# Performance work log

Measured on AMD Instinct MI355X. Metric: run time of the kernel, lower is better.

## Reference

```python
import jax, jax.numpy as jnp
import numpy as np
from jax import lax

IN, H1, H2, F1, OUT = 26, 64, 32, 16, 10
B, T = 512, 1000


def _lstm(x, w_ih, w_hh, b_ih, b_hh):
    """PyTorch-convention LSTM (gate order i,f,g,o). x: [B,T,I].
    Returns (all hidden states [B,T,H], final hidden [B,H])."""
    Bx = x.shape[0]
    H = w_hh.shape[1]
    # Precompute input projections for all timesteps: [B,T,4H]
    xg = jnp.einsum('bti,gi->btg', x, w_ih) + b_ih + b_hh

    def step(carry, xg_t):
        h, c = carry
        gates = xg_t + h @ w_hh.T  # [B,4H]
        i, f, g, o = jnp.split(gates, 4, axis=-1)
        i = jax.nn.sigmoid(i)
        f = jax.nn.sigmoid(f)
        g = jnp.tanh(g)
        o = jax.nn.sigmoid(o)
        c = f * c + i * g
        h = o * jnp.tanh(c)
        return (h, c), h

    init = (jnp.zeros((Bx, H), x.dtype), jnp.zeros((Bx, H), x.dtype))
    (h_last, _), hs = lax.scan(step, init, xg.transpose(1, 0, 2))
    return hs.transpose(1, 0, 2), h_last


def setup_inputs() -> dict:
    key = jax.random.key(0)
    ks = jax.random.split(key, 14)

    def u(k, shape, fan):
        bound = 1.0 / np.sqrt(fan)
        return jax.random.uniform(k, shape, jnp.float32, -bound, bound)

    return {
        'x': jax.random.normal(ks[0], (B, 1, IN, T), jnp.float32),
        'w_ih1': u(ks[1], (4 * H1, IN), H1),
        'w_hh1': u(ks[2], (4 * H1, H1), H1),
        'b_ih1': u(ks[3], (4 * H1,), H1),
        'b_hh1': u(ks[4], (4 * H1,), H1),
        'w_ih2': u(ks[5], (4 * H2, H1), H2),
        'w_hh2': u(ks[6], (4 * H2, H2), H2),
        'b_ih2': u(ks[7], (4 * H2,), H2),
        'b_hh2': u(ks[8], (4 * H2,), H2),
        'w_fc1': u(ks[9], (F1, H2), H2),
        'b_fc1': u(ks[10], (F1,), H2),
        'w_fc2': u(ks[11], (OUT, F1), F1),
        'b_fc2': u(ks[12], (OUT,), F1),
    }


def reference(x, w_ih1, w_hh1, b_ih1, b_hh1, w_ih2, w_hh2, b_ih2, b_hh2,
              w_fc1, b_fc1, w_fc2, b_fc2):
    # [B,1,26,T] -> [B,26,T] -> [B,T,26]
    x = jnp.transpose(x[:, 0], (0, 2, 1))
    out1, _ = _lstm(x, w_ih1, w_hh1, b_ih1, b_hh1)
    # Dropout is identity in eval mode.
    _, h2 = _lstm(out1, w_ih2, w_hh2, b_ih2, b_hh2)  # final hidden [B,32]
    h = jax.nn.relu(h2 @ w_fc1.T + b_fc1)
    return h @ w_fc2.T + b_fc2  # [B,10]
```

## Files before the change

kernel.cpp:

```cpp
#include <hip/hip_runtime.h>
#include <hip/hip_bf16.h>


typedef __hip_bfloat16 bf16;
typedef _Float16 h2v __attribute__((ext_vector_type(2)));

#define T_STEPS 1000
#define IN_DIM  26

__device__ __forceinline__ float bits2f(unsigned short h) {
    unsigned int u = ((unsigned int)h) << 16;
    return __uint_as_float(u);
}

__device__ __forceinline__ float ldv(const void* p, int idx, bool isb) {
    return isb ? bits2f(((const unsigned short*)p)[idx])
               : ((const float*)p)[idx];
}

__device__ __forceinline__ float sigm(float x) {
    return 1.0f / (1.0f + __expf(-x));
}

__device__ __forceinline__ float tanh_(float x) {
    float a = fabsf(x);
    float e = __expf(2.0f * a);
    float r = 1.0f - 2.0f / (e + 1.0f);
    return copysignf(r, x);
}

__device__ __forceinline__ float DOT2(h2v a, h2v b, float c) {
    return __builtin_amdgcn_fdot2(a, b, c, false);
}

__device__ __forceinline__ h2v pkh(float a, float b) {
    h2v r; r[0] = (_Float16)a; r[1] = (_Float16)b; return r;
}

__device__ __forceinline__ h2v f2h2(float f) {
    return __builtin_bit_cast(h2v, f);
}

__global__
__attribute__((amdgpu_flat_work_group_size(128, 128), amdgpu_waves_per_eu(1, 1)))
void lstm_fused(const void* __restrict__ x,
                const void* __restrict__ w_ih1, const void* __restrict__ w_hh1,
                const void* __restrict__ b_ih1, const void* __restrict__ b_hh1,
                const void* __restrict__ w_ih2, const void* __restrict__ w_hh2,
                const void* __restrict__ b_ih2, const void* __restrict__ b_hh2,
                const void* __restrict__ w_fc1, const void* __restrict__ b_fc1,
                const void* __restrict__ w_fc2, const void* __restrict__ b_fc2,
                void* __restrict__ out)
{
    const int j    = threadIdx.x;
    const int wid  = j >> 6;
    const int lane = j & 63;
    const int e    = blockIdx.x;
    const long xbase = (long)e * (IN_DIM * T_STEPS);

    __shared__ __align__(16) _Float16 xsh[2][32];
    __shared__ __align__(16) _Float16 h1sh[2][64];
    __shared__ __align__(16) _Float16 h2sh[32];
    __shared__ __align__(16) float4   xgshf[2][64];
    __shared__ __align__(16) float    f1s[16];

    bool isb = true;
    {
        const unsigned short* wu = (const unsigned short*)w_ih1;
        for (int k = 0; k < 64; ++k) {
            float v = fabsf(bits2f(wu[k]));
            if (!(v <= 0.1251f)) isb = false;
        }
    }

    if (wid == 0) {
        h1sh[0][lane] = (_Float16)0.f;
        h1sh[1][lane] = (_Float16)0.f;

        h2v w1h[4][32];
#pragma unroll
        for (int r = 0; r < 4; ++r) {
            const int row = r * 64 + lane;
#pragma unroll
            for (int q = 0; q < 32; ++q)
                w1h[r][q] = pkh(ldv(w_hh1, row * 64 + 2 * q, isb),
                                ldv(w_hh1, row * 64 + 2 * q + 1, isb));
        }
        __syncthreads();

        float c1 = 0.f;
        for (int s = 0; s <= T_STEPS; ++s) {
            if (s < T_STEPS) {
                const int cur = s & 1, prv = cur ^ 1;
                float4 xg = xgshf[cur][lane];
                float4 hb[8];
                {
                    const float4* hp = (const float4*)h1sh[prv];
#pragma unroll
                    for (int q = 0; q < 8; ++q) hb[q] = hp[q];
                }
                const float* hbf = (const float*)hb;
                float acc[4][2] = {{0.f,0.f},{0.f,0.f},{0.f,0.f},{0.f,0.f}};
#pragma unroll
                for (int q = 0; q < 32; ++q) {
                    h2v hv = f2h2(hbf[q]);
#pragma unroll
                    for (int r = 0; r < 4; ++r)
                        acc[r][q & 1] = DOT2(w1h[r][q], hv, acc[r][q & 1]);
                }
                float pi = acc[0][0] + acc[0][1] + xg.x;
                float pf = acc[1][0] + acc[1][1] + xg.y;
                float pg = acc[2][0] + acc[2][1] + xg.z;
                float po = acc[3][0] + acc[3][1] + xg.w;
                float gi = sigm(pi), gf = sigm(pf), gg = tanh_(pg), go = sigm(po);
                c1 = fmaf(gf, c1, gi * gg);
                h1sh[cur][lane] = (_Float16)(go * tanh_(c1));
            }
            __syncthreads();
        }
    } else {
        h2v w1x[4][13];
        float bias1v[4];
#pragma unroll
        for (int r = 0; r < 4; ++r) {
            const int row = r * 64 + lane;
#pragma unroll
            for (int q = 0; q < 13; ++q)
                w1x[r][q] = pkh(ldv(w_ih1, row * 26 + 2 * q, isb),
                                ldv(w_ih1, row * 26 + 2 * q + 1, isb));
            bias1v[r] = ldv(b_ih1, row, isb) + ldv(b_hh1, row, isb);
        }
        const int u2 = lane & 31;
        const int lo = (lane < 32) ? 1 : 0;
        const int rA2 = (lo ? 0 : 32) + u2;
        const int rB2 = 64 + (lo ? 0 : 32) + u2;
        h2v w2x[2][32], w2h[2][16];
        float bias2v[2];
#pragma unroll
        for (int rr = 0; rr < 2; ++rr) {
            const int row = rr ? rB2 : rA2;
#pragma unroll
            for (int q = 0; q < 32; ++q)
                w2x[rr][q] = pkh(ldv(w_ih2, row * 64 + 2 * q, isb),
                                 ldv(w_ih2, row * 64 + 2 * q + 1, isb));
#pragma unroll
            for (int q = 0; q < 16; ++q)
                w2h[rr][q] = pkh(ldv(w_hh2, row * 32 + 2 * q, isb),
                                 ldv(w_hh2, row * 32 + 2 * q + 1, isb));
            bias2v[rr] = ldv(b_ih2, row, isb) + ldv(b_hh2, row, isb);
        }

        if (lane < 32) {
            h2sh[lane] = (_Float16)0.f;
            xsh[0][lane] = (_Float16)0.f;
            xsh[1][lane] = (_Float16)0.f;
        }
        if (lane < IN_DIM) {
            xsh[0][lane] = (_Float16)ldv(x, xbase + lane * T_STEPS + 0, isb);
            xsh[1][lane] = (_Float16)ldv(x, xbase + lane * T_STEPS + 1, isb);
        }
        {
            float4 xb[4];
            const float4* xp = (const float4*)xsh[0];
#pragma unroll
            for (int q = 0; q < 4; ++q) xb[q] = xp[q];
            const float* xbf = (const float*)xb;
            float ax[4][2] = {{0.f,0.f},{0.f,0.f},{0.f,0.f},{0.f,0.f}};
#pragma unroll
            for (int q = 0; q < 13; ++q) {
                h2v xv = f2h2(xbf[q]);
#pragma unroll
                for (int r = 0; r < 4; ++r)
                    ax[r][q & 1] = DOT2(w1x[r][q], xv, ax[r][q & 1]);
            }
            float4 xg;
            xg.x = ax[0][0] + ax[0][1] + bias1v[0];
            xg.y = ax[1][0] + ax[1][1] + bias1v[1];
            xg.z = ax[2][0] + ax[2][1] + bias1v[2];
            xg.w = ax[3][0] + ax[3][1] + bias1v[3];
            xgshf[0][lane] = xg;
        }
        __syncthreads();

        float c2 = 0.f;
        for (int s = 0; s <= T_STEPS; ++s) {
            float px = 0.f;
            const bool doPf = (s + 2 < T_STEPS) && (lane < IN_DIM);
            if (doPf) px = ldv(x, xbase + lane * T_STEPS + (s + 2), isb);

            if (s + 1 < T_STEPS) {
                const int nb = (s + 1) & 1;
                float4 xb[4];
                const float4* xp = (const float4*)xsh[nb];
#pragma unroll
                for (int q = 0; q < 4; ++q) xb[q] = xp[q];
                const float* xbf = (const float*)xb;
                float ax[4][2] = {{0.f,0.f},{0.f,0.f},{0.f,0.f},{0.f,0.f}};
#pragma unroll
                for (int q = 0; q < 13; ++q) {
                    h2v xv = f2h2(xbf[q]);
#pragma unroll
                    for (int r = 0; r < 4; ++r)
                        ax[r][q & 1] = DOT2(w1x[r][q], xv, ax[r][q & 1]);
                }
                float4 xg;
                xg.x = ax[0][0] + ax[0][1] + bias1v[0];
                xg.y = ax[1][0] + ax[1][1] + bias1v[1];
                xg.z = ax[2][0] + ax[2][1] + bias1v[2];
                xg.w = ax[3][0] + ax[3][1] + bias1v[3];
                xgshf[nb][lane] = xg;
            }

            if (s >= 1) {
                const int hb1 = (s + 1) & 1;
                float4 hb[8];
                {
                    const float4* hp = (const float4*)h1sh[hb1];
#pragma unroll
                    for (int q = 0; q < 8; ++q) hb[q] = hp[q];
                }
                const float* hbf = (const float*)hb;
                float4 pb[4];
                {
                    const float4* pp = (const float4*)h2sh;
#pragma unroll
                    for (int q = 0; q < 4; ++q) pb[q] = pp[q];
                }
                const float* pbf = (const float*)pb;
                float a2[2][2] = {{0.f,0.f},{0.f,0.f}};
#pragma unroll
                for (int q = 0; q < 32; ++q) {
                    h2v hv = f2h2(hbf[q]);
#pragma unroll
                    for (int rr = 0; rr < 2; ++rr)
                        a2[rr][q & 1] = DOT2(w2x[rr][q], hv, a2[rr][q & 1]);
                }
#pragma unroll
                for (int q = 0; q < 16; ++q) {
                    h2v pv = f2h2(pbf[q]);
#pragma unroll
                    for (int rr = 0; rr < 2; ++rr)
                        a2[rr][q & 1] = DOT2(w2h[rr][q], pv, a2[rr][q & 1]);
                }
                float pA = a2[0][0] + a2[0][1] + bias2v[0];
                float pB = a2[1][0] + a2[1][1] + bias2v[1];
                float actA = sigm(pA);
                float actB = lo ? tanh_(pB) : sigm(pB);
                float other = __shfl_xor(
                    __builtin_bit_cast(float, pkh(actA, actB)), 32, 64);
                if (lo) {
                    h2v fo = __builtin_bit_cast(h2v, other);
                    c2 = fmaf((float)fo[0], c2, actA * actB);
                    h2sh[u2] = (_Float16)((float)fo[1] * tanh_(c2));
                }
            }

            if (doPf) xsh[s & 1][lane] = (_Float16)px;

            __syncthreads();
        }

        if (lane < 16) {
            float ss = ldv(b_fc1, lane, isb);
#pragma unroll
            for (int k = 0; k < 32; ++k)
                ss = fmaf(ldv(w_fc1, lane * 32 + k, isb), (float)h2sh[k], ss);
            f1s[lane] = fmaxf(ss, 0.0f);
        }
        if (lane < 10) {
            float ss = ldv(b_fc2, lane, isb);
#pragma unroll
            for (int k = 0; k < 16; ++k)
                ss = fmaf(ldv(w_fc2, lane * 16 + k, isb), f1s[k], ss);
            const int oidx = e * 10 + lane;
            if (isb) ((bf16*)out)[oidx] = __float2bfloat16(ss);
            else     ((float*)out)[oidx] = ss;
        }
    }
}

extern "C" void kernel_launch(void* const* d_in, const int* in_sizes, int n_in,
                              void* d_out, int out_size, void* d_ws, size_t ws_size,
                              hipStream_t stream) {
    lstm_fused<<<dim3(512), dim3(128), 0, stream>>>(
        d_in[0], d_in[1], d_in[2], d_in[3], d_in[4],
        d_in[5], d_in[6], d_in[7], d_in[8],
        d_in[9], d_in[10], d_in[11], d_in[12], d_out);
}
```

Baseline: 913.3 us.

## Batch 16 sequences per block and compute LSTM gates with MFMA

```diff
diff --git a/kernel.cpp b/kernel.cpp
--- a/kernel.cpp
+++ b/kernel.cpp
@@ -3,46 +3,37 @@
 
 
 typedef __hip_bfloat16 bf16;
-typedef _Float16 h2v __attribute__((ext_vector_type(2)));
+typedef _Float16 f16;
+typedef _Float16 f16x8 __attribute__((ext_vector_type(8)));
+typedef _Float16 f16x4 __attribute__((ext_vector_type(4)));
+typedef float    f32x4 __attribute__((ext_vector_type(4)));
 
 #define T_STEPS 1000
 #define IN_DIM  26
+#define EPB     16
+#define CH      16
+#define H1P     72
+#define H2P     40
 
 __device__ __forceinline__ float bits2f(unsigned short h) {
-    unsigned int u = ((unsigned int)h) << 16;
-    return __uint_as_float(u);
-}
-
-__device__ __forceinline__ float ldv(const void* p, int idx, bool isb) {
-    return isb ? bits2f(((const unsigned short*)p)[idx])
-               : ((const float*)p)[idx];
-}
-
+    return __uint_as_float(((unsigned int)h) << 16);
+}
+__device__ __forceinline__ float ldv(const void* p, long i, bool isb) {
+    return isb ? bits2f(((const unsigned short*)p)[i]) : ((const float*)p)[i];
+}
+__device__ __forceinline__ float rcp_(float x) { return __builtin_amdgcn_rcpf(x); }
 __device__ __forceinline__ float sigm(float x) {
-    return 1.0f / (1.0f + __expf(-x));
-}
-
+    return rcp_(1.0f + __expf(-x));
+}
 __device__ __forceinline__ float tanh_(float x) {
     float a = fabsf(x);
-    float e = __expf(2.0f * a);
-    float r = 1.0f - 2.0f / (e + 1.0f);
+    float r = 1.0f - 2.0f * rcp_(__expf(2.0f * a) + 1.0f);
     return copysignf(r, x);
 }
-
-__device__ __forceinline__ float DOT2(h2v a, h2v b, float c) {
-    return __builtin_amdgcn_fdot2(a, b, c, false);
-}
-
-__device__ __forceinline__ h2v pkh(float a, float b) {
-    h2v r; r[0] = (_Float16)a; r[1] = (_Float16)b; return r;
-}
-
-__device__ __forceinline__ h2v f2h2(float f) {
-    return __builtin_bit_cast(h2v, f);
-}
+#define MFMA(a, b, c) __builtin_amdgcn_mfma_f32_16x16x32_f16((a), (b), (c), 0, 0, 0)
 
 __global__
-__attribute__((amdgpu_flat_work_group_size(128, 128), amdgpu_waves_per_eu(1, 1)))
+__attribute__((amdgpu_flat_work_group_size(256, 256), amdgpu_waves_per_eu(1, 1)))
 void lstm_fused(const void* __restrict__ x,
                 const void* __restrict__ w_ih1, const void* __restrict__ w_hh1,
                 const void* __restrict__ b_ih1, const void* __restrict__ b_hh1,
@@ -52,17 +43,17 @@
                 const void* __restrict__ w_fc2, const void* __restrict__ b_fc2,
                 void* __restrict__ out)
 {
-    const int j    = threadIdx.x;
-    const int wid  = j >> 6;
-    const int lane = j & 63;
-    const int e    = blockIdx.x;
-    const long xbase = (long)e * (IN_DIM * T_STEPS);
-
-    __shared__ __align__(16) _Float16 xsh[2][32];
-    __shared__ __align__(16) _Float16 h1sh[2][64];
-    __shared__ __align__(16) _Float16 h2sh[32];
-    __shared__ __align__(16) float4   xgshf[2][64];
-    __shared__ __align__(16) float    f1s[16];
+    const int tid  = threadIdx.x;
+    const int lane = tid & 63;
+    const int wv   = tid >> 6;
+    const int ecol = lane & 15;
+    const int g4   = lane >> 4;
+    const int e0   = blockIdx.x * EPB;
+
+    __shared__ __align__(16) f16  Xst[2][CH][EPB][32];
+    __shared__ __align__(16) f16  H1T[2][EPB][H1P];
+    __shared__ __align__(16) f16  H2T[2][EPB][H2P];
+    __shared__ __align__(16) float f1s[EPB][16];
 
     bool isb = true;
     {
@@ -73,216 +64,171 @@
         }
     }
 
-    if (wid == 0) {
-        h1sh[0][lane] = (_Float16)0.f;
-        h1sh[1][lane] = (_Float16)0.f;
-
-        h2v w1h[4][32];
-#pragma unroll
-        for (int r = 0; r < 4; ++r) {
-            const int row = r * 64 + lane;
-#pragma unroll
-            for (int q = 0; q < 32; ++q)
-                w1h[r][q] = pkh(ldv(w_hh1, row * 64 + 2 * q, isb),
-                                ldv(w_hh1, row * 64 + 2 * q + 1, isb));
-        }
+    {
+        float4 z; z.x = z.y = z.z = z.w = 0.f;
+        float4* p = (float4*)&Xst[0][0][0][0];
+        for (int k = tid; k < (int)(sizeof(Xst) / 16); k += 256) p[k] = z;
+        float4* q = (float4*)&H1T[0][0][0];
+        for (int k = tid; k < (int)(sizeof(H1T) / 16); k += 256) q[k] = z;
+        float4* r = (float4*)&H2T[0][0][0];
+        for (int k = tid; k < (int)(sizeof(H2T) / 16); k += 256) r[k] = z;
+    }
+
+    const int r15 = lane & 15;
+    f16x8 Whh1A[4][2], Wih1A[4];
+    f32x4 b1C[4];
+#pragma unroll
+    for (int gi = 0; gi < 4; ++gi) {
+        const int R = gi * 64 + 16 * wv + r15;
+#pragma unroll
+        for (int k0 = 0; k0 < 2; ++k0)
+#pragma unroll
+            for (int jj = 0; jj < 8; ++jj)
+                Whh1A[gi][k0][jj] =
+                    (f16)ldv(w_hh1, R * 64 + k0 * 32 + g4 * 8 + jj, isb);
+#pragma unroll
+        for (int jj = 0; jj < 8; ++jj) {
+            const int k = g4 * 8 + jj;
+            Wih1A[gi][jj] = (f16)(k < IN_DIM ? ldv(w_ih1, R * IN_DIM + k, isb) : 0.f);
+        }
+#pragma unroll
+        for (int jj = 0; jj < 4; ++jj) {
+            const int Rc = gi * 64 + 16 * wv + g4 * 4 + jj;
+            b1C[gi][jj] = ldv(b_ih1, Rc, isb) + ldv(b_hh1, Rc, isb);
+        }
+    }
+    f16x8 Wih2A[4][2], Whh2A[4];
+    f32x4 b2C[4];
+    if (wv < 2) {
+#pragma unroll
+        for (int gi = 0; gi < 4; ++gi) {
+            const int R = gi * 32 + 16 * wv + r15;
+#pragma unroll
+            for (int k0 = 0; k0 < 2; ++k0)
+#pragma unroll
+                for (int jj = 0; jj < 8; ++jj)
+                    Wih2A[gi][k0][jj] =
+                        (f16)ldv(w_ih2, R * 64 + k0 * 32 + g4 * 8 + jj, isb);
+#pragma unroll
+            for (int jj = 0; jj < 8; ++jj)
+                Whh2A[gi][jj] = (f16)ldv(w_hh2, R * 32 + g4 * 8 + jj, isb);
+#pragma unroll
+            for (int jj = 0; jj < 4; ++jj) {
+                const int Rc = gi * 32 + 16 * wv + g4 * 4 + jj;
+                b2C[gi][jj] = ldv(b_ih2, Rc, isb) + ldv(b_hh2, Rc, isb);
+            }
+        }
+    }
+
+    __syncthreads();
+
+    auto stage = [&](int c) {
+        const int bf = c & 1, t0 = c * CH;
+        const int nt = (T_STEPS - t0 < CH) ? (T_STEPS - t0) : CH;
+        for (int p = tid; p < EPB * IN_DIM; p += 256) {
+            const int e = p / IN_DIM, i = p - e * IN_DIM;
+            const long gb = ((long)(e0 + e) * IN_DIM + i) * T_STEPS + t0;
+            for (int t = 0; t < nt; ++t)
+                Xst[bf][t][e][i] = (f16)ldv(x, gb + t, isb);
+        }
+    };
+    stage(0);
+    __syncthreads();
+
+    f32x4 xgc[4];
+    {
+        const f16x8 xf = *(const f16x8*)&Xst[0][0][ecol][g4 * 8];
+#pragma unroll
+        for (int gi = 0; gi < 4; ++gi) xgc[gi] = MFMA(Wih1A[gi], xf, b1C[gi]);
+    }
+
+    float c1[4] = {0.f, 0.f, 0.f, 0.f};
+    float c2[4] = {0.f, 0.f, 0.f, 0.f};
+
+    for (int s = 0; s <= T_STEPS; ++s) {
+        const int pc = s & 1, pp = pc ^ 1;
+        const f16x8 h1f0 = *(const f16x8*)&H1T[pp][ecol][g4 * 8];
+        const f16x8 h1f1 = *(const f16x8*)&H1T[pp][ecol][32 + g4 * 8];
+
+        if (s < T_STEPS) {
+            f32x4 gt[4];
+#pragma unroll
+            for (int gi = 0; gi < 4; ++gi) {
+                f32x4 t0 = MFMA(Whh1A[gi][0], h1f0, xgc[gi]);
+                gt[gi]   = MFMA(Whh1A[gi][1], h1f1, t0);
+            }
+            if (s + 1 < T_STEPS) {
+                const int sn = s + 1;
+                const f16x8 xf =
+                    *(const f16x8*)&Xst[(sn >> 4) & 1][sn & 15][ecol][g4 * 8];
+#pragma unroll
+                for (int gi = 0; gi < 4; ++gi) xgc[gi] = MFMA(Wih1A[gi], xf, b1C[gi]);
+            }
+            f16x4 hh;
+#pragma unroll
+            for (int jj = 0; jj < 4; ++jj) {
+                const float ii = sigm(gt[0][jj]);
+                const float ff = sigm(gt[1][jj]);
+                const float gg = tanh_(gt[2][jj]);
+                const float oo = sigm(gt[3][jj]);
+                c1[jj] = fmaf(ff, c1[jj], ii * gg);
+                hh[jj] = (f16)(oo * tanh_(c1[jj]));
+            }
+            *(f16x4*)&H1T[pc][ecol][16 * wv + g4 * 4] = hh;
+        }
+
+        if (wv < 2 && s >= 1) {
+            const f16x8 h2f = *(const f16x8*)&H2T[pc][ecol][g4 * 8];
+            f32x4 gt[4];
+#pragma unroll
+            for (int gi = 0; gi < 4; ++gi) {
+                f32x4 t0 = MFMA(Wih2A[gi][0], h1f0, b2C[gi]);
+                t0       = MFMA(Wih2A[gi][1], h1f1, t0);
+                gt[gi]   = MFMA(Whh2A[gi], h2f, t0);
+            }
+            f16x4 hh;
+#pragma unroll
+            for (int jj = 0; jj < 4; ++jj) {
+                const float ii = sigm(gt[0][jj]);
+                const float ff = sigm(gt[1][jj]);
+                const float gg = tanh_(gt[2][jj]);
+                const float oo = sigm(gt[3][jj]);
+                c2[jj] = fmaf(ff, c2[jj], ii * gg);
+                hh[jj] = (f16)(oo * tanh_(c2[jj]));
+            }
+            *(f16x4*)&H2T[pp][ecol][16 * wv + g4 * 4] = hh;
+        }
+
+        if ((s & (CH - 1)) == 0 && s + CH < T_STEPS) stage((s >> 4) + 1);
+
         __syncthreads();
-
-        float c1 = 0.f;
-        for (int s = 0; s <= T_STEPS; ++s) {
-            if (s < T_STEPS) {
-                const int cur = s & 1, prv = cur ^ 1;
-                float4 xg = xgshf[cur][lane];
-                float4 hb[8];
-                {
-                    const float4* hp = (const float4*)h1sh[prv];
-#pragma unroll
-                    for (int q = 0; q < 8; ++q) hb[q] = hp[q];
-                }
-                const float* hbf = (const float*)hb;
-                float acc[4][2] = {{0.f,0.f},{0.f,0.f},{0.f,0.f},{0.f,0.f}};
-#pragma unroll
-                for (int q = 0; q < 32; ++q) {
-                    h2v hv = f2h2(hbf[q]);
-#pragma unroll
-                    for (int r = 0; r < 4; ++r)
-                        acc[r][q & 1] = DOT2(w1h[r][q], hv, acc[r][q & 1]);
-                }
-                float pi = acc[0][0] + acc[0][1] + xg.x;
-                float pf = acc[1][0] + acc[1][1] + xg.y;
-                float pg = acc[2][0] + acc[2][1] + xg.z;
-                float po = acc[3][0] + acc[3][1] + xg.w;
-                float gi = sigm(pi), gf = sigm(pf), gg = tanh_(pg), go = sigm(po);
-                c1 = fmaf(gf, c1, gi * gg);
-                h1sh[cur][lane] = (_Float16)(go * tanh_(c1));
-            }
-            __syncthreads();
-        }
-    } else {
-        h2v w1x[4][13];
-        float bias1v[4];
-#pragma unroll
-        for (int r = 0; r < 4; ++r) {
-            const int row = r * 64 + lane;
-#pragma unroll
-            for (int q = 0; q < 13; ++q)
-                w1x[r][q] = pkh(ldv(w_ih1, row * 26 + 2 * q, isb),
-                                ldv(w_ih1, row * 26 + 2 * q + 1, isb));
-            bias1v[r] = ldv(b_ih1, row, isb) + ldv(b_hh1, row, isb);
-        }
-        const int u2 = lane & 31;
-        const int lo = (lane < 32) ? 1 : 0;
-        const int rA2 = (lo ? 0 : 32) + u2;
-        const int rB2 = 64 + (lo ? 0 : 32) + u2;
-        h2v w2x[2][32], w2h[2][16];
-        float bias2v[2];
-#pragma unroll
-        for (int rr = 0; rr < 2; ++rr) {
-            const int row = rr ? rB2 : rA2;
-#pragma unroll
-            for (int q = 0; q < 32; ++q)
-                w2x[rr][q] = pkh(ldv(w_ih2, row * 64 + 2 * q, isb),
-                                 ldv(w_ih2, row * 64 + 2 * q + 1, isb));
-#pragma unroll
-            for (int q = 0; q < 16; ++q)
-                w2h[rr][q] = pkh(ldv(w_hh2, row * 32 + 2 * q, isb),
-                                 ldv(w_hh2, row * 32 + 2 * q + 1, isb));
-            bias2v[rr] = ldv(b_ih2, row, isb) + ldv(b_hh2, row, isb);
-        }
-
-        if (lane < 32) {
-            h2sh[lane] = (_Float16)0.f;
-            xsh[0][lane] = (_Float16)0.f;
-            xsh[1][lane] = (_Float16)0.f;
-        }
-        if (lane < IN_DIM) {
-            xsh[0][lane] = (_Float16)ldv(x, xbase + lane * T_STEPS + 0, isb);
-            xsh[1][lane] = (_Float16)ldv(x, xbase + lane * T_STEPS + 1, isb);
-        }
-        {
-            float4 xb[4];
-            const float4* xp = (const float4*)xsh[0];
-#pragma unroll
-            for (int q = 0; q < 4; ++q) xb[q] = xp[q];
-            const float* xbf = (const float*)xb;
-            float ax[4][2] = {{0.f,0.f},{0.f,0.f},{0.f,0.f},{0.f,0.f}};
-#pragma unroll
-            for (int q = 0; q < 13; ++q) {
-                h2v xv = f2h2(xbf[q]);
-#pragma unroll
-                for (int r = 0; r < 4; ++r)
-                    ax[r][q & 1] = DOT2(w1x[r][q], xv, ax[r][q & 1]);
-            }
-            float4 xg;
-            xg.x = ax[0][0] + ax[0][1] + bias1v[0];
-            xg.y = ax[1][0] + ax[1][1] + bias1v[1];
-            xg.z = ax[2][0] + ax[2][1] + bias1v[2];
-            xg.w = ax[3][0] + ax[3][1] + bias1v[3];
-            xgshf[0][lane] = xg;
-        }
-        __syncthreads();
-
-        float c2 = 0.f;
-        for (int s = 0; s <= T_STEPS; ++s) {
-            float px = 0.f;
-            const bool doPf = (s + 2 < T_STEPS) && (lane < IN_DIM);
-            if (doPf) px = ldv(x, xbase + lane * T_STEPS + (s + 2), isb);
-
-            if (s + 1 < T_STEPS) {
-                const int nb = (s + 1) & 1;
-                float4 xb[4];
-                const float4* xp = (const float4*)xsh[nb];
-#pragma unroll
-                for (int q = 0; q < 4; ++q) xb[q] = xp[q];
-                const float* xbf = (const float*)xb;
-                float ax[4][2] = {{0.f,0.f},{0.f,0.f},{0.f,0.f},{0.f,0.f}};
-#pragma unroll
-                for (int q = 0; q < 13; ++q) {
-                    h2v xv = f2h2(xbf[q]);
-#pragma unroll
-                    for (int r = 0; r < 4; ++r)
-                        ax[r][q & 1] = DOT2(w1x[r][q], xv, ax[r][q & 1]);
-                }
-                float4 xg;
-                xg.x = ax[0][0] + ax[0][1] + bias1v[0];
-                xg.y = ax[1][0] + ax[1][1] + bias1v[1];
-                xg.z = ax[2][0] + ax[2][1] + bias1v[2];
-                xg.w = ax[3][0] + ax[3][1] + bias1v[3];
-                xgshf[nb][lane] = xg;
-            }
-
-            if (s >= 1) {
-                const int hb1 = (s + 1) & 1;
-                float4 hb[8];
-                {
-                    const float4* hp = (const float4*)h1sh[hb1];
-#pragma unroll
-                    for (int q = 0; q < 8; ++q) hb[q] = hp[q];
-                }
-                const float* hbf = (const float*)hb;
-                float4 pb[4];
-                {
-                    const float4* pp = (const float4*)h2sh;
-#pragma unroll
-                    for (int q = 0; q < 4; ++q) pb[q] = pp[q];
-                }
-                const float* pbf = (const float*)pb;
-                float a2[2][2] = {{0.f,0.f},{0.f,0.f}};
-#pragma unroll
-                for (int q = 0; q < 32; ++q) {
-                    h2v hv = f2h2(hbf[q]);
-#pragma unroll
-                    for (int rr = 0; rr < 2; ++rr)
-                        a2[rr][q & 1] = DOT2(w2x[rr][q], hv, a2[rr][q & 1]);
-                }
-#pragma unroll
-                for (int q = 0; q < 16; ++q) {
-                    h2v pv = f2h2(pbf[q]);
-#pragma unroll
-                    for (int rr = 0; rr < 2; ++rr)
-                        a2[rr][q & 1] = DOT2(w2h[rr][q], pv, a2[rr][q & 1]);
-                }
-                float pA = a2[0][0] + a2[0][1] + bias2v[0];
-                float pB = a2[1][0] + a2[1][1] + bias2v[1];
-                float actA = sigm(pA);
-                float actB = lo ? tanh_(pB) : sigm(pB);
-                float other = __shfl_xor(
-                    __builtin_bit_cast(float, pkh(actA, actB)), 32, 64);
-                if (lo) {
-                    h2v fo = __builtin_bit_cast(h2v, other);
-                    c2 = fmaf((float)fo[0], c2, actA * actB);
-                    h2sh[u2] = (_Float16)((float)fo[1] * tanh_(c2));
-                }
-            }
-
-            if (doPf) xsh[s & 1][lane] = (_Float16)px;
-
-            __syncthreads();
-        }
-
-        if (lane < 16) {
-            float ss = ldv(b_fc1, lane, isb);
-#pragma unroll
-            for (int k = 0; k < 32; ++k)
-                ss = fmaf(ldv(w_fc1, lane * 32 + k, isb), (float)h2sh[k], ss);
-            f1s[lane] = fmaxf(ss, 0.0f);
-        }
-        if (lane < 10) {
-            float ss = ldv(b_fc2, lane, isb);
-#pragma unroll
-            for (int k = 0; k < 16; ++k)
-                ss = fmaf(ldv(w_fc2, lane * 16 + k, isb), f1s[k], ss);
-            const int oidx = e * 10 + lane;
-            if (isb) ((bf16*)out)[oidx] = __float2bfloat16(ss);
-            else     ((float*)out)[oidx] = ss;
-        }
+    }
+
+    {
+        const int e = tid >> 4, o = tid & 15;
+        float ss = ldv(b_fc1, o, isb);
+#pragma unroll 8
+        for (int k = 0; k < 32; ++k)
+            ss = fmaf(ldv(w_fc1, o * 32 + k, isb), (float)H2T[1][e][k], ss);
+        f1s[e][o] = fmaxf(ss, 0.f);
+    }
+    __syncthreads();
+    if (tid < EPB * 10) {
+        const int e = tid / 10, o = tid - e * 10;
+        float ss = ldv(b_fc2, o, isb);
+#pragma unroll
+        for (int k = 0; k < 16; ++k)
+            ss = fmaf(ldv(w_fc2, o * 16 + k, isb), f1s[e][k], ss);
+        const long oi = (long)(e0 + e) * 10 + o;
+        if (isb) ((bf16*)out)[oi] = __float2bfloat16(ss);
+        else     ((float*)out)[oi] = ss;
     }
 }
 
 extern "C" void kernel_launch(void* const* d_in, const int* in_sizes, int n_in,
                               void* d_out, int out_size, void* d_ws, size_t ws_size,
                               hipStream_t stream) {
-    lstm_fused<<<dim3(512), dim3(128), 0, stream>>>(
+    lstm_fused<<<dim3(512 / EPB), dim3(256), 0, stream>>>(
         d_in[0], d_in[1], d_in[2], d_in[3], d_in[4],
         d_in[5], d_in[6], d_in[7], d_in[8],
         d_in[9], d_in[10], d_in[11], d_in[12], d_out);
```

Result: slower. 1.508 ms (+65.1%).
